# Kernel tuning notes

Measured on AMD Instinct MI355X. Metric: run time of the kernel, lower is better.

The kernel has to match this reference:

```python
import jax, jax.numpy as jnp
import numpy as np

B, LATENT, P, NUM_ATOMS, H, L, E = 16, 128, 16, 64, 64, 4, 32768
N = P * NUM_ATOMS  # 1024

def _lin(k, i, o, s=0.05):
    kw, kb = jax.random.split(k)
    return jax.random.normal(kw, (i, o), jnp.float32) * s, jax.random.normal(kb, (o,), jnp.float32) * s

def setup_inputs() -> dict:
    key = jax.random.key(0)
    ks = jax.random.split(key, 32)
    z = jax.random.normal(ks[0], (B, LATENT), jnp.float32)
    edge_index = jax.random.randint(ks[1], (2, E), 0, N, jnp.int32)
    # build_node_features: (frame/P, atom/num_atoms, 1) per node
    fr = jnp.repeat(jnp.arange(P), NUM_ATOMS) / P
    at = jnp.tile(jnp.arange(NUM_ATOMS), P) / NUM_ATOMS
    node_features = jnp.stack([fr, at, jnp.ones(N)], -1).astype(jnp.float32)
    Wg, bg = _lin(ks[2], LATENT, H)
    Wn, bn = _lin(ks[3], 3, H)
    def stack(fn, base):
        outs = [fn(jax.random.fold_in(key, base + l)) for l in range(L)]
        return tuple(jnp.stack(t) for t in zip(*outs))
    eW1, eb1 = stack(lambda k: _lin(k, 2 * H + 1, H), 100)
    eW2, eb2 = stack(lambda k: _lin(k, H, H), 200)
    cW1, cb1 = stack(lambda k: _lin(k, H, H), 300)
    cW2 = jnp.stack([jax.random.normal(jax.random.fold_in(key, 400 + l), (H, 1), jnp.float32) * 0.05 for l in range(L)])
    nW1, nb1 = stack(lambda k: _lin(k, 2 * H, H), 500)
    nW2, nb2 = stack(lambda k: _lin(k, H, H), 600)
    lng = jnp.ones((L, H), jnp.float32)
    lnb = jnp.zeros((L, H), jnp.float32)
    oW1, ob1 = _lin(ks[4], H, H)
    oW2, ob2 = _lin(ks[5], H, 3)
    return dict(z=z, edge_index=edge_index, node_features=node_features, Wg=Wg, bg=bg, Wn=Wn, bn=bn,
                eW1=eW1, eb1=eb1, eW2=eW2, eb2=eb2, cW1=cW1, cb1=cb1, cW2=cW2,
                nW1=nW1, nb1=nb1, nW2=nW2, nb2=nb2, lng=lng, lnb=lnb,
                oW1=oW1, ob1=ob1, oW2=oW2, ob2=ob2)

def _forward(z, edge_index, node_features, Wg, bg, Wn, bn, eW1, eb1, eW2, eb2,
             cW1, cb1, cW2, nW1, nb1, nW2, nb2, lng, lnb, oW1, ob1, oW2, ob2):
    b = z.shape[0]
    n = node_features.shape[0]
    row, col = edge_index[0], edge_index[1]  # aggregate messages to row
    counts = jnp.clip(jnp.zeros((n,), jnp.float32).at[row].add(1.0), 1.0, None)
    g = z @ Wg + bg                              # [B,H]
    h = (node_features @ Wn + bn)[None] + g[:, None]  # [B,N,H]
    pos = jnp.zeros((b, n, 3), h.dtype)
    for l in range(L):
        hi, hj = h[:, row], h[:, col]            # [B,E,H] gathers
        diff = pos[:, row] - pos[:, col]         # [B,E,3]
        d2 = jnp.sum(diff * diff, -1, keepdims=True)
        m = jax.nn.silu(jnp.concatenate([hi, hj, d2], -1) @ eW1[l] + eb1[l])
        m = jax.nn.silu(m @ eW2[l] + eb2[l])     # [B,E,H]
        w = jax.nn.silu(m @ cW1[l] + cb1[l]) @ cW2[l]  # [B,E,1]
        trans = diff * w
        pos = pos + jnp.zeros_like(pos).at[:, row].add(trans) / counts[None, :, None]
        agg = jnp.zeros_like(h).at[:, row].add(m)      # scatter-sum to nodes
        u = jax.nn.silu(jnp.concatenate([h, agg], -1) @ nW1[l] + nb1[l]) @ nW2[l] + nb2[l]
        h = h + u                                 # node residual
        mu = jnp.mean(h, -1, keepdims=True)
        var = jnp.mean((h - mu) ** 2, -1, keepdims=True)
        h = (h - mu) * jax.lax.rsqrt(var + 1e-5) * lng[l] + lnb[l]
    out = jax.nn.relu(h @ oW1 + ob1) @ oW2 + ob2   # [B,N,3]
    return out.reshape(b, -1)

def reference(z, edge_index, node_features, Wg, bg, Wn, bn, eW1, eb1, eW2, eb2,
              cW1, cb1, cW2, nW1, nb1, nW2, nb2, lng, lnb, oW1, ob1, oW2, ob2):
    return _forward(z, edge_index, node_features, Wg, bg, Wn, bn, eW1, eb1, eW2, eb2,
                    cW1, cb1, cW2, nW1, nb1, nW2, nb2, lng, lnb, oW1, ob1, oW2, ob2)
```

## Files before the change

### kernel.cpp

```cpp
#include <hip/hip_runtime.h>
#include <hip/hip_bf16.h>


namespace {

constexpr int kE = 32768, kLat = 128;

typedef __attribute__((ext_vector_type(8))) short short8;
typedef __attribute__((ext_vector_type(4))) float floatx4;

__device__ __forceinline__ unsigned short f2bf(float f){
  union { float f; unsigned int u; } v; v.f = f;
  unsigned int r = v.u + 0x7fffu + ((v.u >> 16) & 1u);
  return (unsigned short)(r >> 16);
}
__device__ __forceinline__ unsigned int packbf(float a, float b){
  return ((unsigned int)f2bf(b) << 16) | (unsigned int)f2bf(a);
}
__device__ __forceinline__ unsigned int pack2f(float a, float b){
  unsigned int ua = __float_as_uint(a) + 0x8000u;
  unsigned int ub = __float_as_uint(b) + 0x8000u;
  return __builtin_amdgcn_perm(ub, ua, 0x07060302);
}
__device__ __forceinline__ float bflo(unsigned int u){
  union { unsigned int u; float f; } v; v.u = u << 16; return v.f;
}
__device__ __forceinline__ float bfhi(unsigned int u){
  union { unsigned int u; float f; } v; v.u = u & 0xffff0000u; return v.f;
}
__device__ __forceinline__ float silu2(float x){
  float u = __builtin_amdgcn_exp2f(-1.44269504f * x);
  return x * __builtin_amdgcn_rcpf(1.0f + u);
}

__device__ __forceinline__ void gemm16g(const float* __restrict__ Wg,
                                        const float* Xl,
                                        int j0, int r0, float acc[4][4]){
  #pragma unroll 4
  for (int k = 0; k < 64; k++){
    float4 w = *(const float4*)(Wg + k*64 + j0);
    float4 x = *(const float4*)(Xl + k*20 + r0);
    float xv[4] = { x.x, x.y, x.z, x.w };
    float wv[4] = { w.x, w.y, w.z, w.w };
    #pragma unroll
    for (int i = 0; i < 4; i++)
      #pragma unroll
      for (int j = 0; j < 4; j++)
        acc[i][j] += xv[i]*wv[j];
  }
}

__global__ void k_scancnt(const int* ei, int* off, int* fill,
                          const float* z, const float* Wg, const float* bg,
                          float* g){
  __shared__ int s0[1024];
  __shared__ int s1[1024];
  int t = threadIdx.x;
  s0[t] = 0; fill[t] = 0;
  __syncthreads();
  #pragma unroll
  for (int i = 0; i < 32; i++) atomicAdd(&s0[ei[i*1024 + t]], 1);
  __syncthreads();
  int c = s0[t];
  int* src = s0; int* dst = s1;
  for (int o = 1; o < 1024; o <<= 1){
    int v = src[t] + ((t >= o) ? src[t-o] : 0);
    dst[t] = v; __syncthreads();
    int* tmp = src; src = dst; dst = tmp;
  }
  int inc = src[t];
  off[t] = inc - c;
  if (t == 1023) off[1024] = inc;
  int b = t >> 6, j = t & 63;
  float acc = bg[j];
  for (int k = 0; k < kLat; k++) acc += z[b*kLat + k] * Wg[k*64 + j];
  g[b*64 + j] = acc;
}

__global__ void k_bucket(const int* ei, const int* off, int* fill, int* ecol,
                         const float* eW2, unsigned short* wfragE,
                         const float* nf, const float* Wn, const float* bn,
                         const float* eW1, const float* eb1, const float* g,
                         float* An1, float* An2, float* Ag1, float* Ag2){
  __shared__ __align__(16) float W0[4096];
  __shared__ __align__(16) float W1[4096];
  __shared__ __align__(16) float HR[16*68];
  int tid = threadIdx.x, bid = blockIdx.x;
  int e = bid*256 + tid;
  int r = ei[e];
  int s = atomicAdd(&fill[r], 1);
  ecol[off[r] + s] = ei[kE + e];
  if (bid < 4){
    int l = bid;
    for (int i = tid; i < 4096; i += 256){
      int f = i >> 9, lane = (i >> 3) & 63, j8 = i & 7;
      int jt = f >> 1, ks = f & 1;
      int k = ks*32 + (lane >> 4)*8 + j8;
      int j = jt*16 + (lane & 15);
      wfragE[l*4096 + i] = f2bf(eW2[l*4096 + k*64 + j]);
    }
  } else if (bid < 68){
    const float4* e1a = (const float4*)(eW1);
    const float4* e1b = (const float4*)(eW1 + 4096);
    for (int i = tid; i < 1024; i += 256){
      ((float4*)W0)[i] = e1a[i]; ((float4*)W1)[i] = e1b[i];
    }
    int rl = tid >> 4, c = tid & 15, j0 = c*4;
    int n = (bid - 4)*16 + rl;
    float f0 = nf[n*3], f1 = nf[n*3+1], f2 = nf[n*3+2];
    float4 hv;
    hv.x = f0*Wn[j0+0] + f1*Wn[64+j0+0] + f2*Wn[128+j0+0] + bn[j0+0];
    hv.y = f0*Wn[j0+1] + f1*Wn[64+j0+1] + f2*Wn[128+j0+1] + bn[j0+1];
    hv.z = f0*Wn[j0+2] + f1*Wn[64+j0+2] + f2*Wn[128+j0+2] + bn[j0+2];
    hv.w = f0*Wn[j0+3] + f1*Wn[64+j0+3] + f2*Wn[128+j0+3] + bn[j0+3];
    *(float4*)(HR + rl*68 + j0) = hv;
    __syncthreads();
    float4 b1 = *(const float4*)(eb1 + j0);
    float a1[4] = { b1.x, b1.y, b1.z, b1.w };
    float a2[4] = { 0.f, 0.f, 0.f, 0.f };
    #pragma unroll 8
    for (int k = 0; k < 64; k++){
      float hk = HR[rl*68 + k];
      float4 w1 = *(const float4*)(W0 + k*64 + j0);
      float4 w2 = *(const float4*)(W1 + k*64 + j0);
      a1[0] += hk*w1.x; a1[1] += hk*w1.y; a1[2] += hk*w1.z; a1[3] += hk*w1.w;
      a2[0] += hk*w2.x; a2[1] += hk*w2.y; a2[2] += hk*w2.z; a2[3] += hk*w2.w;
    }
    float4 o1 = { a1[0], a1[1], a1[2], a1[3] };
    float4 o2 = { a2[0], a2[1], a2[2], a2[3] };
    *(float4*)(An1 + n*64 + j0) = o1;
    *(float4*)(An2 + n*64 + j0) = o2;
  } else if (bid == 68){
    int bb = tid >> 4, j0 = (tid & 15)*4;
    float a1[4] = {0.f,0.f,0.f,0.f}, a2[4] = {0.f,0.f,0.f,0.f};
    for (int k = 0; k < 64; k++){
      float gk = g[bb*64 + k];
      float4 w1 = *(const float4*)(eW1 + k*64 + j0);
      float4 w2 = *(const float4*)(eW1 + 4096 + k*64 + j0);
      a1[0] += gk*w1.x; a1[1] += gk*w1.y; a1[2] += gk*w1.z; a1[3] += gk*w1.w;
      a2[0] += gk*w2.x; a2[1] += gk*w2.y; a2[2] += gk*w2.z; a2[3] += gk*w2.w;
    }
    float4 o1 = { a1[0], a1[1], a1[2], a1[3] };
    float4 o2 = { a2[0], a2[1], a2[2], a2[3] };
    *(float4*)(Ag1 + bb*64 + j0) = o1;
    *(float4*)(Ag2 + bb*64 + j0) = o2;
  }
}

__global__ __launch_bounds__(256, 1) void k_pre1(const float* nf, const float* Wn,
      const float* bn, const float* g, const float* An1, const float* An2,
      const float* Ag1, const float* Ag2, float* h, float* A1,
      unsigned short* A2){
  int idx = blockIdx.x*256 + threadIdx.x;
  int row = idx >> 4;
  int j0  = (idx & 15) * 4;
  int n = row >> 4, bb = row & 15;
  float4 a1 = *(const float4*)(An1 + n*64 + j0);
  float4 g1 = *(const float4*)(Ag1 + bb*64 + j0);
  a1.x += g1.x; a1.y += g1.y; a1.z += g1.z; a1.w += g1.w;
  *(float4*)(A1 + row*64 + j0) = a1;
  float4 a2 = *(const float4*)(An2 + n*64 + j0);
  float4 g2 = *(const float4*)(Ag2 + bb*64 + j0);
  a2.x += g2.x; a2.y += g2.y; a2.z += g2.z; a2.w += g2.w;
  uint2 pk; pk.x = packbf(a2.x, a2.y); pk.y = packbf(a2.z, a2.w);
  *(uint2*)(A2 + row*64 + j0) = pk;
  float f0 = nf[n*3], f1 = nf[n*3+1], f2 = nf[n*3+2];
  float4 w0 = *(const float4*)(Wn + j0);
  float4 w1 = *(const float4*)(Wn + 64 + j0);
  float4 w2 = *(const float4*)(Wn + 128 + j0);
  float4 bv = *(const float4*)(bn + j0);
  float4 gv = *(const float4*)(g + bb*64 + j0);
  float4 hv;
  hv.x = f0*w0.x + f1*w1.x + f2*w2.x + bv.x + gv.x;
  hv.y = f0*w0.y + f1*w1.y + f2*w2.y + bv.y + gv.y;
  hv.z = f0*w0.z + f1*w1.z + f2*w2.z + bv.z + gv.z;
  hv.w = f0*w0.w + f1*w1.w + f2*w2.w + bv.w + gv.w;
  *(float4*)(h + (bb*1024 + n)*64 + j0) = hv;
}

template <bool LAST>
__global__ __launch_bounds__(256) void k_layer(int l,
      const float* A1r, const unsigned short* A2r,
      float* A1w, unsigned short* A2w,
      float* h, const unsigned short* wfragE, const float* eb2,
      const int* off, const int* ecol,
      const float* nW1, const float* nb1_, const float* nW2, const float* nb2_,
      const float* lng_, const float* lnb_, const float* eW1, const float* eb1_,
      const float* oW1, const float* ob1_, const float* oW2, const float* ob2_,
      float* out){
  __shared__ __align__(16) float XT[64*20];
  __shared__ __align__(16) float AGL[64*20];
  int tid = threadIdx.x, nd = blockIdx.x;
  int lane = tid & 63, wv = tid >> 6, m = lane & 15, quad = lane >> 4;

  for (int i = tid; i < 64*20; i += 256) AGL[i] = 0.f;
  __syncthreads();

  {
    short8 wf[8];
    #pragma unroll
    for (int f = 0; f < 8; f++)
      wf[f] = *(const short8*)(wfragE + l*4096 + f*512 + lane*8);
    floatx4 dini[4], agg[4];
    #pragma unroll
    for (int jt = 0; jt < 4; jt++){
      dini[jt] = *(const floatx4*)(eb2 + l*64 + jt*16 + quad*4);
      agg[jt] = (floatx4){0.f,0.f,0.f,0.f};
    }
    int e0 = off[nd] + wv, e1 = off[nd+1];
    if (e0 < e1){
      float4 a1[4];
      #pragma unroll
      for (int ks = 0; ks < 2; ks++){
        a1[ks*2+0] = *(const float4*)(A1r + (nd<<10) + (m<<6) + ks*32 + quad*8);
        a1[ks*2+1] = *(const float4*)(A1r + (nd<<10) + (m<<6) + ks*32 + quad*8 + 4);
      }
      int c0 = ecol[e0];
      uint4 p0 = *(const uint4*)(A2r + ((c0<<4)+m)*64 + quad*8);
      uint4 p1 = *(const uint4*)(A2r + ((c0<<4)+m)*64 + 32 + quad*8);
      for (int e = e0; e < e1; e += 4){
        uint4 c_0 = p0, c_1 = p1;
        if (e + 4 < e1){
          int cn = ecol[e+4];
          p0 = *(const uint4*)(A2r + ((cn<<4)+m)*64 + quad*8);
          p1 = *(const uint4*)(A2r + ((cn<<4)+m)*64 + 32 + quad*8);
        }
        short8 bfr[2];
        #pragma unroll
        for (int ks = 0; ks < 2; ks++){
          uint4 a2r = (ks == 0) ? c_0 : c_1;
          float4 x0 = a1[ks*2+0];
          float4 x1 = a1[ks*2+1];
          float v0 = silu2(x0.x + bflo(a2r.x));
          float v1 = silu2(x0.y + bfhi(a2r.x));
          float v2 = silu2(x0.z + bflo(a2r.y));
          float v3 = silu2(x0.w + bfhi(a2r.y));
          float v4 = silu2(x1.x + bflo(a2r.z));
          float v5 = silu2(x1.y + bfhi(a2r.z));
          float v6 = silu2(x1.z + bflo(a2r.w));
          float v7 = silu2(x1.w + bfhi(a2r.w));
          union { uint4 u; short8 s; } bu;
          bu.u.x = pack2f(v0, v1); bu.u.y = pack2f(v2, v3);
          bu.u.z = pack2f(v4, v5); bu.u.w = pack2f(v6, v7);
          bfr[ks] = bu.s;
        }
        #pragma unroll
        for (int jt = 0; jt < 4; jt++){
          floatx4 d = dini[jt];
          d = __builtin_amdgcn_mfma_f32_16x16x32_bf16(wf[jt*2+0], bfr[0], d, 0, 0, 0);
          d = __builtin_amdgcn_mfma_f32_16x16x32_bf16(wf[jt*2+1], bfr[1], d, 0, 0, 0);
          floatx4 a = agg[jt];
          a.x += silu2(d.x); a.y += silu2(d.y);
          a.z += silu2(d.z); a.w += silu2(d.w);
          agg[jt] = a;
        }
      }
    }
    #pragma unroll
    for (int jt = 0; jt < 4; jt++)
      #pragma unroll
      for (int i = 0; i < 4; i++)
        atomicAdd(&AGL[(jt*16 + quad*4 + i)*20 + m], agg[jt][i]);
  }
  __syncthreads();
  if (wv != 0) return;

  int c = tid & 15, gq = (tid >> 4) & 3;
  int j0 = c*4, r0 = gq*4;

  float hold[4][4];
  float acc[4][4];
  #pragma unroll
  for (int i = 0; i < 4; i++){
    int bb = r0 + i;
    float4 v = *(const float4*)(h + (bb*1024 + nd)*64 + j0);
    hold[i][0]=v.x; hold[i][1]=v.y; hold[i][2]=v.z; hold[i][3]=v.w;
  }
  #pragma unroll
  for (int j = 0; j < 4; j++){
    float4 t = { hold[0][j], hold[1][j], hold[2][j], hold[3][j] };
    *(float4*)(XT + (j0 + j)*20 + r0) = t;
  }
  { float4 b1 = *(const float4*)(nb1_ + l*64 + j0);
    float bv[4] = { b1.x, b1.y, b1.z, b1.w };
    #pragma unroll
    for (int i = 0; i < 4; i++)
      #pragma unroll
      for (int j = 0; j < 4; j++) acc[i][j] = bv[j]; }
  gemm16g(nW1 + l*8192, XT, j0, r0, acc);
  gemm16g(nW1 + l*8192 + 4096, AGL, j0, r0, acc);
  #pragma unroll
  for (int i = 0; i < 4; i++)
    #pragma unroll
    for (int j = 0; j < 4; j++) acc[i][j] = silu2(acc[i][j]);
  #pragma unroll
  for (int j = 0; j < 4; j++){
    float4 t = { acc[0][j], acc[1][j], acc[2][j], acc[3][j] };
    *(float4*)(XT + (j0 + j)*20 + r0) = t;
  }
  float u4[4][4];
  { float4 b2 = *(const float4*)(nb2_ + l*64 + j0);
    float bv[4] = { b2.x, b2.y, b2.z, b2.w };
    #pragma unroll
    for (int i = 0; i < 4; i++)
      #pragma unroll
      for (int j = 0; j < 4; j++) u4[i][j] = bv[j]; }
  gemm16g(nW2 + l*4096, XT, j0, r0, u4);
  float4 lgv = *(const float4*)(lng_ + l*64 + j0);
  float4 lbv = *(const float4*)(lnb_ + l*64 + j0);
  float hn[4][4];
  #pragma unroll
  for (int i = 0; i < 4; i++){
    float hv[4];
    #pragma unroll
    for (int j = 0; j < 4; j++) hv[j] = hold[i][j] + u4[i][j];
    float s1 = hv[0]+hv[1]+hv[2]+hv[3];
    float s2 = hv[0]*hv[0]+hv[1]*hv[1]+hv[2]*hv[2]+hv[3]*hv[3];
    s1 += __shfl_xor(s1, 1, 64); s1 += __shfl_xor(s1, 2, 64);
    s1 += __shfl_xor(s1, 4, 64); s1 += __shfl_xor(s1, 8, 64);
    s2 += __shfl_xor(s2, 1, 64); s2 += __shfl_xor(s2, 2, 64);
    s2 += __shfl_xor(s2, 4, 64); s2 += __shfl_xor(s2, 8, 64);
    float mu  = s1 * (1.0f/64.0f);
    float var = s2 * (1.0f/64.0f) - mu*mu;
    float rs  = rsqrtf(var + 1e-5f);
    hn[i][0] = (hv[0]-mu)*rs*lgv.x + lbv.x;
    hn[i][1] = (hv[1]-mu)*rs*lgv.y + lbv.y;
    hn[i][2] = (hv[2]-mu)*rs*lgv.z + lbv.z;
    hn[i][3] = (hv[3]-mu)*rs*lgv.w + lbv.w;
  }
  if (!LAST){
    #pragma unroll
    for (int i = 0; i < 4; i++){
      int bb = r0 + i;
      float4 v = { hn[i][0], hn[i][1], hn[i][2], hn[i][3] };
      *(float4*)(h + (bb*1024 + nd)*64 + j0) = v;
    }
    #pragma unroll
    for (int j = 0; j < 4; j++){
      float4 t = { hn[0][j], hn[1][j], hn[2][j], hn[3][j] };
      *(float4*)(XT + (j0 + j)*20 + r0) = t;
    }
    float a1r[4][4];
    { float4 b1 = *(const float4*)(eb1_ + (l+1)*64 + j0);
      float bv[4] = { b1.x, b1.y, b1.z, b1.w };
      #pragma unroll
      for (int i = 0; i < 4; i++)
        #pragma unroll
        for (int j = 0; j < 4; j++) a1r[i][j] = bv[j]; }
    gemm16g(eW1 + (l+1)*8256, XT, j0, r0, a1r);
    float a2r[4][4];
    #pragma unroll
    for (int i = 0; i < 4; i++)
      #pragma unroll
      for (int j = 0; j < 4; j++) a2r[i][j] = 0.f;
    gemm16g(eW1 + (l+1)*8256 + 4096, XT, j0, r0, a2r);
    #pragma unroll
    for (int i = 0; i < 4; i++){
      int bb = r0 + i;
      int tb = (nd*16 + bb)*64 + j0;
      float4 o1 = { a1r[i][0], a1r[i][1], a1r[i][2], a1r[i][3] };
      *(float4*)(A1w + tb) = o1;
      uint2 pk; pk.x = packbf(a2r[i][0], a2r[i][1]);
      pk.y = packbf(a2r[i][2], a2r[i][3]);
      *(uint2*)(A2w + tb) = pk;
    }
  } else {
    #pragma unroll
    for (int j = 0; j < 4; j++){
      float4 t = { hn[0][j], hn[1][j], hn[2][j], hn[3][j] };
      *(float4*)(XT + (j0 + j)*20 + r0) = t;
    }
    float tr[4][4];
    { float4 b1 = *(const float4*)(ob1_ + j0);
      float bv[4] = { b1.x, b1.y, b1.z, b1.w };
      #pragma unroll
      for (int i = 0; i < 4; i++)
        #pragma unroll
        for (int j = 0; j < 4; j++) tr[i][j] = bv[j]; }
    gemm16g(oW1, XT, j0, r0, tr);
    #pragma unroll
    for (int i = 0; i < 4; i++)
      #pragma unroll
      for (int j = 0; j < 4; j++) tr[i][j] = fmaxf(tr[i][j], 0.f);
    float po[4][3];
    #pragma unroll
    for (int i = 0; i < 4; i++){ po[i][0]=0.f; po[i][1]=0.f; po[i][2]=0.f; }
    #pragma unroll
    for (int j = 0; j < 4; j++){
      float w0 = oW2[(j0+j)*3 + 0];
      float w1 = oW2[(j0+j)*3 + 1];
      float w2 = oW2[(j0+j)*3 + 2];
      #pragma unroll
      for (int i = 0; i < 4; i++){
        po[i][0] += tr[i][j]*w0;
        po[i][1] += tr[i][j]*w1;
        po[i][2] += tr[i][j]*w2;
      }
    }
    #pragma unroll
    for (int i = 0; i < 4; i++)
      #pragma unroll
      for (int uu = 0; uu < 3; uu++){
        float v = po[i][uu];
        v += __shfl_xor(v, 1, 64); v += __shfl_xor(v, 2, 64);
        v += __shfl_xor(v, 4, 64); v += __shfl_xor(v, 8, 64);
        po[i][uu] = v;
      }
    if (c == 0){
      #pragma unroll
      for (int i = 0; i < 4; i++){
        int bb = r0 + i;
        out[bb*3072 + nd*3 + 0] = po[i][0] + ob2_[0];
        out[bb*3072 + nd*3 + 1] = po[i][1] + ob2_[1];
        out[bb*3072 + nd*3 + 2] = po[i][2] + ob2_[2];
      }
    }
  }
}

}

extern "C" void kernel_launch(void* const* d_in, const int* in_sizes, int n_in,
                              void* d_out, int out_size, void* d_ws, size_t ws_size,
                              hipStream_t stream){
  const float* z   = (const float*)d_in[0];
  const int*   ei  = (const int*)d_in[1];
  const float* nf  = (const float*)d_in[2];
  const float* Wg  = (const float*)d_in[3];  const float* bg  = (const float*)d_in[4];
  const float* Wn  = (const float*)d_in[5];  const float* bn  = (const float*)d_in[6];
  const float* eW1 = (const float*)d_in[7];  const float* eb1 = (const float*)d_in[8];
  const float* eW2 = (const float*)d_in[9];  const float* eb2 = (const float*)d_in[10];
  const float* nW1 = (const float*)d_in[14]; const float* nb1 = (const float*)d_in[15];
  const float* nW2 = (const float*)d_in[16]; const float* nb2 = (const float*)d_in[17];
  const float* lng = (const float*)d_in[18]; const float* lnb = (const float*)d_in[19];
  const float* oW1 = (const float*)d_in[20]; const float* ob1 = (const float*)d_in[21];
  const float* oW2 = (const float*)d_in[22]; const float* ob2 = (const float*)d_in[23];

  float* W      = (float*)d_ws;
  float* h      = W;
  float* A1a    = W + 1048576;
  float* A1b    = W + 2097152;
  unsigned short* A2a    = (unsigned short*)(W + 3145728);
  unsigned short* A2b    = (unsigned short*)(W + 3670016);
  unsigned short* wfragE = (unsigned short*)(W + 4194304);
  float* g      = W + 4202496;
  float* An1    = W + 4203520;
  float* An2    = W + 4269056;
  float* Ag1    = W + 4334592;
  float* Ag2    = W + 4335616;
  int*   off    = (int*)(W + 4336640);
  int*   fill   = off + 1025;
  int*   ecol   = fill + 1024;

  k_scancnt<<<1, 1024, 0, stream>>>(ei, off, fill, z, Wg, bg, g);
  k_bucket <<<128, 256, 0, stream>>>(ei, off, fill, ecol, eW2, wfragE,
                                     nf, Wn, bn, eW1, eb1, g, An1, An2, Ag1, Ag2);
  k_pre1   <<<1024,256, 0, stream>>>(nf, Wn, bn, g, An1, An2, Ag1, Ag2, h, A1a, A2a);

  for (int l = 0; l < 4; l++){
    const float* A1r = (l & 1) ? A1b : A1a;
    const unsigned short* A2r = (l & 1) ? A2b : A2a;
    float* A1w = (l & 1) ? A1a : A1b;
    unsigned short* A2w = (l & 1) ? A2a : A2b;
    if (l < 3)
      k_layer<false><<<1024, 256, 0, stream>>>(l, A1r, A2r, A1w, A2w, h, wfragE,
            eb2, off, ecol, nW1, nb1, nW2, nb2, lng, lnb, eW1, eb1,
            oW1, ob1, oW2, ob2, (float*)d_out);
    else
      k_layer<true> <<<1024, 256, 0, stream>>>(l, A1r, A2r, A1w, A2w, h, wfragE,
            eb2, off, ecol, nW1, nb1, nW2, nb2, lng, lnb, eW1, eb1,
            oW1, ob1, oW2, ob2, (float*)d_out);
  }
}
```

Baseline: 390.9 us.

## Spread node-update tail across all four wavefronts, one batch row per lane group

Previously only wavefront 0 ran the per-node MLP, layernorm and next-layer projection tail, each lane computing a 4x4 tile while the other waves exited. Now every wavefront takes part: each lane group owns one batch row (row = wave*4 + group) and computes a 1x4 output slice. This removes the serial tail where three quarters of the block sat idle. In exchange each lane reloads the weight float4 for every single row, so there is less register reuse and more weight-load traffic per FLOP.

```diff
diff --git a/kernel.cpp b/kernel.cpp
--- a/kernel.cpp
+++ b/kernel.cpp
@@ -33,20 +33,14 @@
   return x * __builtin_amdgcn_rcpf(1.0f + u);
 }
 
-__device__ __forceinline__ void gemm16g(const float* __restrict__ Wg,
-                                        const float* Xl,
-                                        int j0, int r0, float acc[4][4]){
+__device__ __forceinline__ void gemmR(const float* __restrict__ Wg,
+                                      const float* Xl, int j0, int row,
+                                      float acc[4]){
   #pragma unroll 4
   for (int k = 0; k < 64; k++){
     float4 w = *(const float4*)(Wg + k*64 + j0);
-    float4 x = *(const float4*)(Xl + k*20 + r0);
-    float xv[4] = { x.x, x.y, x.z, x.w };
-    float wv[4] = { w.x, w.y, w.z, w.w };
-    #pragma unroll
-    for (int i = 0; i < 4; i++)
-      #pragma unroll
-      for (int j = 0; j < 4; j++)
-        acc[i][j] += xv[i]*wv[j];
+    float x = Xl[k*20 + row];
+    acc[0] += x*w.x; acc[1] += x*w.y; acc[2] += x*w.z; acc[3] += x*w.w;
   }
 }
 
@@ -263,57 +257,38 @@
         atomicAdd(&AGL[(jt*16 + quad*4 + i)*20 + m], agg[jt][i]);
   }
   __syncthreads();
-  if (wv != 0) return;
-
-  int c = tid & 15, gq = (tid >> 4) & 3;
-  int j0 = c*4, r0 = gq*4;
-
-  float hold[4][4];
-  float acc[4][4];
+
+  int c = lane & 15, gq = (lane >> 4) & 3;
+  int j0 = c*4;
+  int row = wv*4 + gq;
+
+  float hold[4];
+  {
+    float4 v = *(const float4*)(h + (row*1024 + nd)*64 + j0);
+    hold[0]=v.x; hold[1]=v.y; hold[2]=v.z; hold[3]=v.w;
+  }
   #pragma unroll
-  for (int i = 0; i < 4; i++){
-    int bb = r0 + i;
-    float4 v = *(const float4*)(h + (bb*1024 + nd)*64 + j0);
-    hold[i][0]=v.x; hold[i][1]=v.y; hold[i][2]=v.z; hold[i][3]=v.w;
-  }
+  for (int jj = 0; jj < 4; jj++) XT[(j0 + jj)*20 + row] = hold[jj];
+  float acc[4];
+  { float4 b1 = *(const float4*)(nb1_ + l*64 + j0);
+    acc[0]=b1.x; acc[1]=b1.y; acc[2]=b1.z; acc[3]=b1.w; }
+  gemmR(nW1 + l*8192, XT, j0, row, acc);
+  gemmR(nW1 + l*8192 + 4096, AGL, j0, row, acc);
   #pragma unroll
-  for (int j = 0; j < 4; j++){
-    float4 t = { hold[0][j], hold[1][j], hold[2][j], hold[3][j] };
-    *(float4*)(XT + (j0 + j)*20 + r0) = t;
-  }
-  { float4 b1 = *(const float4*)(nb1_ + l*64 + j0);
-    float bv[4] = { b1.x, b1.y, b1.z, b1.w };
-    #pragma unroll
-    for (int i = 0; i < 4; i++)
-      #pragma unroll
-      for (int j = 0; j < 4; j++) acc[i][j] = bv[j]; }
-  gemm16g(nW1 + l*8192, XT, j0, r0, acc);
-  gemm16g(nW1 + l*8192 + 4096, AGL, j0, r0, acc);
+  for (int jj = 0; jj < 4; jj++) acc[jj] = silu2(acc[jj]);
   #pragma unroll
-  for (int i = 0; i < 4; i++)
-    #pragma unroll
-    for (int j = 0; j < 4; j++) acc[i][j] = silu2(acc[i][j]);
-  #pragma unroll
-  for (int j = 0; j < 4; j++){
-    float4 t = { acc[0][j], acc[1][j], acc[2][j], acc[3][j] };
-    *(float4*)(XT + (j0 + j)*20 + r0) = t;
-  }
-  float u4[4][4];
+  for (int jj = 0; jj < 4; jj++) XT[(j0 + jj)*20 + row] = acc[jj];
+  float u4[4];
   { float4 b2 = *(const float4*)(nb2_ + l*64 + j0);
-    float bv[4] = { b2.x, b2.y, b2.z, b2.w };
-    #pragma unroll
-    for (int i = 0; i < 4; i++)
-      #pragma unroll
-      for (int j = 0; j < 4; j++) u4[i][j] = bv[j]; }
-  gemm16g(nW2 + l*4096, XT, j0, r0, u4);
+    u4[0]=b2.x; u4[1]=b2.y; u4[2]=b2.z; u4[3]=b2.w; }
+  gemmR(nW2 + l*4096, XT, j0, row, u4);
   float4 lgv = *(const float4*)(lng_ + l*64 + j0);
   float4 lbv = *(const float4*)(lnb_ + l*64 + j0);
-  float hn[4][4];
-  #pragma unroll
-  for (int i = 0; i < 4; i++){
+  float hn[4];
+  {
     float hv[4];
     #pragma unroll
-    for (int j = 0; j < 4; j++) hv[j] = hold[i][j] + u4[i][j];
+    for (int jj = 0; jj < 4; jj++) hv[jj] = hold[jj] + u4[jj];
     float s1 = hv[0]+hv[1]+hv[2]+hv[3];
     float s2 = hv[0]*hv[0]+hv[1]*hv[1]+hv[2]*hv[2]+hv[3]*hv[3];
     s1 += __shfl_xor(s1, 1, 64); s1 += __shfl_xor(s1, 2, 64);
@@ -323,97 +298,56 @@
     float mu  = s1 * (1.0f/64.0f);
     float var = s2 * (1.0f/64.0f) - mu*mu;
     float rs  = rsqrtf(var + 1e-5f);
-    hn[i][0] = (hv[0]-mu)*rs*lgv.x + lbv.x;
-    hn[i][1] = (hv[1]-mu)*rs*lgv.y + lbv.y;
-    hn[i][2] = (hv[2]-mu)*rs*lgv.z + lbv.z;
-    hn[i][3] = (hv[3]-mu)*rs*lgv.w + lbv.w;
+    hn[0] = (hv[0]-mu)*rs*lgv.x + lbv.x;
+    hn[1] = (hv[1]-mu)*rs*lgv.y + lbv.y;
+    hn[2] = (hv[2]-mu)*rs*lgv.z + lbv.z;
+    hn[3] = (hv[3]-mu)*rs*lgv.w + lbv.w;
   }
   if (!LAST){
-    #pragma unroll
-    for (int i = 0; i < 4; i++){
-      int bb = r0 + i;
-      float4 v = { hn[i][0], hn[i][1], hn[i][2], hn[i][3] };
-      *(float4*)(h + (bb*1024 + nd)*64 + j0) = v;
-    }
-    #pragma unroll
-    for (int j = 0; j < 4; j++){
-      float4 t = { hn[0][j], hn[1][j], hn[2][j], hn[3][j] };
-      *(float4*)(XT + (j0 + j)*20 + r0) = t;
-    }
-    float a1r[4][4];
+    { float4 v = { hn[0], hn[1], hn[2], hn[3] };
+      *(float4*)(h + (row*1024 + nd)*64 + j0) = v; }
+    #pragma unroll
+    for (int jj = 0; jj < 4; jj++) XT[(j0 + jj)*20 + row] = hn[jj];
+    float a1r[4];
     { float4 b1 = *(const float4*)(eb1_ + (l+1)*64 + j0);
-      float bv[4] = { b1.x, b1.y, b1.z, b1.w };
-      #pragma unroll
-      for (int i = 0; i < 4; i++)
-        #pragma unroll
-        for (int j = 0; j < 4; j++) a1r[i][j] = bv[j]; }
-    gemm16g(eW1 + (l+1)*8256, XT, j0, r0, a1r);
-    float a2r[4][4];
-    #pragma unroll
-    for (int i = 0; i < 4; i++)
-      #pragma unroll
-      for (int j = 0; j < 4; j++) a2r[i][j] = 0.f;
-    gemm16g(eW1 + (l+1)*8256 + 4096, XT, j0, r0, a2r);
-    #pragma unroll
-    for (int i = 0; i < 4; i++){
-      int bb = r0 + i;
-      int tb = (nd*16 + bb)*64 + j0;
-      float4 o1 = { a1r[i][0], a1r[i][1], a1r[i][2], a1r[i][3] };
-      *(float4*)(A1w + tb) = o1;
-      uint2 pk; pk.x = packbf(a2r[i][0], a2r[i][1]);
-      pk.y = packbf(a2r[i][2], a2r[i][3]);
-      *(uint2*)(A2w + tb) = pk;
-    }
+      a1r[0]=b1.x; a1r[1]=b1.y; a1r[2]=b1.z; a1r[3]=b1.w; }
+    gemmR(eW1 + (l+1)*8256, XT, j0, row, a1r);
+    float a2r[4] = { 0.f, 0.f, 0.f, 0.f };
+    gemmR(eW1 + (l+1)*8256 + 4096, XT, j0, row, a2r);
+    int tb = (nd*16 + row)*64 + j0;
+    float4 o1 = { a1r[0], a1r[1], a1r[2], a1r[3] };
+    *(float4*)(A1w + tb) = o1;
+    uint2 pk; pk.x = packbf(a2r[0], a2r[1]);
+    pk.y = packbf(a2r[2], a2r[3]);
+    *(uint2*)(A2w + tb) = pk;
   } else {
     #pragma unroll
-    for (int j = 0; j < 4; j++){
-      float4 t = { hn[0][j], hn[1][j], hn[2][j], hn[3][j] };
-      *(float4*)(XT + (j0 + j)*20 + r0) = t;
-    }
-    float tr[4][4];
+    for (int jj = 0; jj < 4; jj++) XT[(j0 + jj)*20 + row] = hn[jj];
+    float tr[4];
     { float4 b1 = *(const float4*)(ob1_ + j0);
-      float bv[4] = { b1.x, b1.y, b1.z, b1.w };
-      #pragma unroll
-      for (int i = 0; i < 4; i++)
-        #pragma unroll
-        for (int j = 0; j < 4; j++) tr[i][j] = bv[j]; }
-    gemm16g(oW1, XT, j0, r0, tr);
-    #pragma unroll
-    for (int i = 0; i < 4; i++)
-      #pragma unroll
-      for (int j = 0; j < 4; j++) tr[i][j] = fmaxf(tr[i][j], 0.f);
-    float po[4][3];
-    #pragma unroll
-    for (int i = 0; i < 4; i++){ po[i][0]=0.f; po[i][1]=0.f; po[i][2]=0.f; }
-    #pragma unroll
-    for (int j = 0; j < 4; j++){
-      float w0 = oW2[(j0+j)*3 + 0];
-      float w1 = oW2[(j0+j)*3 + 1];
-      float w2 = oW2[(j0+j)*3 + 2];
-      #pragma unroll
-      for (int i = 0; i < 4; i++){
-        po[i][0] += tr[i][j]*w0;
-        po[i][1] += tr[i][j]*w1;
-        po[i][2] += tr[i][j]*w2;
-      }
-    }
-    #pragma unroll
-    for (int i = 0; i < 4; i++)
-      #pragma unroll
-      for (int uu = 0; uu < 3; uu++){
-        float v = po[i][uu];
-        v += __shfl_xor(v, 1, 64); v += __shfl_xor(v, 2, 64);
-        v += __shfl_xor(v, 4, 64); v += __shfl_xor(v, 8, 64);
-        po[i][uu] = v;
-      }
+      tr[0]=b1.x; tr[1]=b1.y; tr[2]=b1.z; tr[3]=b1.w; }
+    gemmR(oW1, XT, j0, row, tr);
+    #pragma unroll
+    for (int jj = 0; jj < 4; jj++) tr[jj] = fmaxf(tr[jj], 0.f);
+    float po[3] = { 0.f, 0.f, 0.f };
+    #pragma unroll
+    for (int jj = 0; jj < 4; jj++){
+      float w0 = oW2[(j0+jj)*3 + 0];
+      float w1 = oW2[(j0+jj)*3 + 1];
+      float w2 = oW2[(j0+jj)*3 + 2];
+      po[0] += tr[jj]*w0; po[1] += tr[jj]*w1; po[2] += tr[jj]*w2;
+    }
+    #pragma unroll
+    for (int uu = 0; uu < 3; uu++){
+      float v = po[uu];
+      v += __shfl_xor(v, 1, 64); v += __shfl_xor(v, 2, 64);
+      v += __shfl_xor(v, 4, 64); v += __shfl_xor(v, 8, 64);
+      po[uu] = v;
+    }
     if (c == 0){
-      #pragma unroll
-      for (int i = 0; i < 4; i++){
-        int bb = r0 + i;
-        out[bb*3072 + nd*3 + 0] = po[i][0] + ob2_[0];
-        out[bb*3072 + nd*3 + 1] = po[i][1] + ob2_[1];
-        out[bb*3072 + nd*3 + 2] = po[i][2] + ob2_[2];
-      }
+      out[row*3072 + nd*3 + 0] = po[0] + ob2_[0];
+      out[row*3072 + nd*3 + 1] = po[1] + ob2_[1];
+      out[row*3072 + nd*3 + 2] = po[2] + ob2_[2];
     }
   }
 }
```

Result: slower. 501.8 us (+28.4%).

## Split layer kernel into edge and node-update kernels with LDS-staged weights

Applied to the files above, without the earlier changes.

The fused per-node layer kernel is split into an edge-aggregation kernel that writes per-node aggregates to a global buffer, and a node-update kernel that processes four nodes per block with all 256 threads. The node kernel stages each 64x64 weight matrix into shared memory and reuses it across 64 rows, where previously one wave per node read the weights from global memory. This is meant to raise weight reuse and thread utilisation in the node MLP, layernorm and next-layer projection. The cost is an extra launch per layer, a global round trip for the aggregates, and more barriers and shared memory.

```diff
diff --git a/kernel.cpp b/kernel.cpp
--- a/kernel.cpp
+++ b/kernel.cpp
@@ -33,13 +33,20 @@
   return x * __builtin_amdgcn_rcpf(1.0f + u);
 }
 
-__device__ __forceinline__ void gemm16g(const float* __restrict__ Wg,
-                                        const float* Xl,
-                                        int j0, int r0, float acc[4][4]){
+__device__ __forceinline__ void stage16k(float* Wl, const float* src, int tid){
+  const float4* p = (const float4*)src;
+  float4* d = (float4*)Wl;
+  d[tid]       = p[tid];
+  d[tid + 256] = p[tid + 256];
+  d[tid + 512] = p[tid + 512];
+  d[tid + 768] = p[tid + 768];
+}
+__device__ __forceinline__ void gemm64(const float* Wl, const float* Xl,
+                                       int j0, int r0, float acc[4][4]){
   #pragma unroll 4
   for (int k = 0; k < 64; k++){
-    float4 w = *(const float4*)(Wg + k*64 + j0);
-    float4 x = *(const float4*)(Xl + k*20 + r0);
+    float4 w = *(const float4*)(Wl + k*64 + j0);
+    float4 x = *(const float4*)(Xl + k*68 + r0);
     float xv[4] = { x.x, x.y, x.z, x.w };
     float wv[4] = { w.x, w.y, w.z, w.w };
     #pragma unroll
@@ -178,24 +185,16 @@
   *(float4*)(h + (bb*1024 + n)*64 + j0) = hv;
 }
 
-template <bool LAST>
-__global__ __launch_bounds__(256) void k_layer(int l,
+__global__ __launch_bounds__(256) void k_edge(int l,
       const float* A1r, const unsigned short* A2r,
-      float* A1w, unsigned short* A2w,
-      float* h, const unsigned short* wfragE, const float* eb2,
-      const int* off, const int* ecol,
-      const float* nW1, const float* nb1_, const float* nW2, const float* nb2_,
-      const float* lng_, const float* lnb_, const float* eW1, const float* eb1_,
-      const float* oW1, const float* ob1_, const float* oW2, const float* ob2_,
-      float* out){
-  __shared__ __align__(16) float XT[64*20];
+      const unsigned short* wfragE, const float* eb2,
+      const int* off, const int* ecol, float* AG){
   __shared__ __align__(16) float AGL[64*20];
   int tid = threadIdx.x, nd = blockIdx.x;
   int lane = tid & 63, wv = tid >> 6, m = lane & 15, quad = lane >> 4;
 
   for (int i = tid; i < 64*20; i += 256) AGL[i] = 0.f;
   __syncthreads();
-
   {
     short8 wf[8];
     #pragma unroll
@@ -263,32 +262,61 @@
         atomicAdd(&AGL[(jt*16 + quad*4 + i)*20 + m], agg[jt][i]);
   }
   __syncthreads();
-  if (wv != 0) return;
-
-  int c = tid & 15, gq = (tid >> 4) & 3;
+  int f = tid >> 2, b4 = (tid & 3) * 4;
+  float4 v = *(const float4*)(AGL + f*20 + b4);
+  *(float4*)(AG + nd*1024 + f*16 + b4) = v;
+}
+
+template <bool LAST>
+__global__ __launch_bounds__(256) void k_post(int l,
+      const float* AG, float* h, float* A1w, unsigned short* A2w,
+      const float* nW1, const float* nb1_, const float* nW2, const float* nb2_,
+      const float* lng_, const float* lnb_, const float* eW1, const float* eb1_,
+      const float* oW1, const float* ob1_, const float* oW2, const float* ob2_,
+      float* out){
+  __shared__ __align__(16) float W[4096];
+  __shared__ __align__(16) float XT[64*68];
+  __shared__ __align__(16) float AGT[64*68];
+  __shared__ float W2o[192];
+  __shared__ float ob2s[4];
+  int tid = threadIdx.x, bid = blockIdx.x;
+  int n0 = bid * 4;
+  int c = tid & 15, gq = tid >> 4;
   int j0 = c*4, r0 = gq*4;
 
-  float hold[4][4];
+  stage16k(W, nW1 + l*8192, tid);
+  for (int i = tid; i < 1024; i += 256){
+    int f4 = i >> 6, rr = i & 63;
+    int q = rr >> 4, b = rr & 15;
+    float4 v = *(const float4*)(h + (b*1024 + n0 + q)*64 + f4*4);
+    XT[(f4*4+0)*68 + rr] = v.x;
+    XT[(f4*4+1)*68 + rr] = v.y;
+    XT[(f4*4+2)*68 + rr] = v.z;
+    XT[(f4*4+3)*68 + rr] = v.w;
+  }
+  for (int i = tid; i < 1024; i += 256){
+    int q = i >> 8, j = i & 255, f = j >> 2, b4 = (j & 3)*4;
+    float4 v = *(const float4*)(AG + (n0+q)*1024 + f*16 + b4);
+    *(float4*)(AGT + f*68 + q*16 + b4) = v;
+  }
   float acc[4][4];
-  #pragma unroll
-  for (int i = 0; i < 4; i++){
-    int bb = r0 + i;
-    float4 v = *(const float4*)(h + (bb*1024 + nd)*64 + j0);
-    hold[i][0]=v.x; hold[i][1]=v.y; hold[i][2]=v.z; hold[i][3]=v.w;
-  }
-  #pragma unroll
-  for (int j = 0; j < 4; j++){
-    float4 t = { hold[0][j], hold[1][j], hold[2][j], hold[3][j] };
-    *(float4*)(XT + (j0 + j)*20 + r0) = t;
-  }
   { float4 b1 = *(const float4*)(nb1_ + l*64 + j0);
     float bv[4] = { b1.x, b1.y, b1.z, b1.w };
     #pragma unroll
     for (int i = 0; i < 4; i++)
       #pragma unroll
       for (int j = 0; j < 4; j++) acc[i][j] = bv[j]; }
-  gemm16g(nW1 + l*8192, XT, j0, r0, acc);
-  gemm16g(nW1 + l*8192 + 4096, AGL, j0, r0, acc);
+  __syncthreads();
+  gemm64(W, XT, j0, r0, acc);
+  float hold[4][4];
+  #pragma unroll
+  for (int i = 0; i < 4; i++)
+    #pragma unroll
+    for (int j = 0; j < 4; j++) hold[i][j] = XT[(j0+j)*68 + r0+i];
+  __syncthreads();
+  stage16k(W, nW1 + l*8192 + 4096, tid);
+  __syncthreads();
+  gemm64(W, AGT, j0, r0, acc);
   #pragma unroll
   for (int i = 0; i < 4; i++)
     #pragma unroll
@@ -296,8 +324,11 @@
   #pragma unroll
   for (int j = 0; j < 4; j++){
     float4 t = { acc[0][j], acc[1][j], acc[2][j], acc[3][j] };
-    *(float4*)(XT + (j0 + j)*20 + r0) = t;
-  }
+    *(float4*)(XT + (j0 + j)*68 + r0) = t;
+  }
+  __syncthreads();
+  stage16k(W, nW2 + l*4096, tid);
+  __syncthreads();
   float u4[4][4];
   { float4 b2 = *(const float4*)(nb2_ + l*64 + j0);
     float bv[4] = { b2.x, b2.y, b2.z, b2.w };
@@ -305,7 +336,7 @@
     for (int i = 0; i < 4; i++)
       #pragma unroll
       for (int j = 0; j < 4; j++) u4[i][j] = bv[j]; }
-  gemm16g(nW2 + l*4096, XT, j0, r0, u4);
+  gemm64(W, XT, j0, r0, u4);
   float4 lgv = *(const float4*)(lng_ + l*64 + j0);
   float4 lbv = *(const float4*)(lnb_ + l*64 + j0);
   float hn[4][4];
@@ -328,17 +359,20 @@
     hn[i][2] = (hv[2]-mu)*rs*lgv.z + lbv.z;
     hn[i][3] = (hv[3]-mu)*rs*lgv.w + lbv.w;
   }
+  __syncthreads();
   if (!LAST){
+    stage16k(W, eW1 + (l+1)*8256, tid);
     #pragma unroll
     for (int i = 0; i < 4; i++){
-      int bb = r0 + i;
+      int rr = r0 + i;
+      int q = rr >> 4, b = rr & 15;
       float4 v = { hn[i][0], hn[i][1], hn[i][2], hn[i][3] };
-      *(float4*)(h + (bb*1024 + nd)*64 + j0) = v;
+      *(float4*)(h + (b*1024 + n0 + q)*64 + j0) = v;
     }
     #pragma unroll
     for (int j = 0; j < 4; j++){
       float4 t = { hn[0][j], hn[1][j], hn[2][j], hn[3][j] };
-      *(float4*)(XT + (j0 + j)*20 + r0) = t;
+      *(float4*)(XT + (j0 + j)*68 + r0) = t;
     }
     float a1r[4][4];
     { float4 b1 = *(const float4*)(eb1_ + (l+1)*64 + j0);
@@ -347,17 +381,22 @@
       for (int i = 0; i < 4; i++)
         #pragma unroll
         for (int j = 0; j < 4; j++) a1r[i][j] = bv[j]; }
-    gemm16g(eW1 + (l+1)*8256, XT, j0, r0, a1r);
+    __syncthreads();
+    gemm64(W, XT, j0, r0, a1r);
+    __syncthreads();
+    stage16k(W, eW1 + (l+1)*8256 + 4096, tid);
     float a2r[4][4];
     #pragma unroll
     for (int i = 0; i < 4; i++)
       #pragma unroll
       for (int j = 0; j < 4; j++) a2r[i][j] = 0.f;
-    gemm16g(eW1 + (l+1)*8256 + 4096, XT, j0, r0, a2r);
+    __syncthreads();
+    gemm64(W, XT, j0, r0, a2r);
     #pragma unroll
     for (int i = 0; i < 4; i++){
-      int bb = r0 + i;
-      int tb = (nd*16 + bb)*64 + j0;
+      int rr = r0 + i;
+      int q = rr >> 4, b = rr & 15;
+      int tb = ((n0+q)*16 + b)*64 + j0;
       float4 o1 = { a1r[i][0], a1r[i][1], a1r[i][2], a1r[i][3] };
       *(float4*)(A1w + tb) = o1;
       uint2 pk; pk.x = packbf(a2r[i][0], a2r[i][1]);
@@ -365,10 +404,13 @@
       *(uint2*)(A2w + tb) = pk;
     }
   } else {
+    stage16k(W, oW1, tid);
+    if (tid < 192) W2o[tid] = oW2[tid];
+    if (tid < 3)   ob2s[tid] = ob2_[tid];
     #pragma unroll
     for (int j = 0; j < 4; j++){
       float4 t = { hn[0][j], hn[1][j], hn[2][j], hn[3][j] };
-      *(float4*)(XT + (j0 + j)*20 + r0) = t;
+      *(float4*)(XT + (j0 + j)*68 + r0) = t;
     }
     float tr[4][4];
     { float4 b1 = *(const float4*)(ob1_ + j0);
@@ -377,7 +419,8 @@
       for (int i = 0; i < 4; i++)
         #pragma unroll
         for (int j = 0; j < 4; j++) tr[i][j] = bv[j]; }
-    gemm16g(oW1, XT, j0, r0, tr);
+    __syncthreads();
+    gemm64(W, XT, j0, r0, tr);
     #pragma unroll
     for (int i = 0; i < 4; i++)
       #pragma unroll
@@ -387,9 +430,9 @@
     for (int i = 0; i < 4; i++){ po[i][0]=0.f; po[i][1]=0.f; po[i][2]=0.f; }
     #pragma unroll
     for (int j = 0; j < 4; j++){
-      float w0 = oW2[(j0+j)*3 + 0];
-      float w1 = oW2[(j0+j)*3 + 1];
-      float w2 = oW2[(j0+j)*3 + 2];
+      float w0 = W2o[(j0+j)*3 + 0];
+      float w1 = W2o[(j0+j)*3 + 1];
+      float w2 = W2o[(j0+j)*3 + 2];
       #pragma unroll
       for (int i = 0; i < 4; i++){
         po[i][0] += tr[i][j]*w0;
@@ -409,10 +452,11 @@
     if (c == 0){
       #pragma unroll
       for (int i = 0; i < 4; i++){
-        int bb = r0 + i;
-        out[bb*3072 + nd*3 + 0] = po[i][0] + ob2_[0];
-        out[bb*3072 + nd*3 + 1] = po[i][1] + ob2_[1];
-        out[bb*3072 + nd*3 + 2] = po[i][2] + ob2_[2];
+        int rr = r0 + i;
+        int q = rr >> 4, b = rr & 15;
+        out[b*3072 + (n0+q)*3 + 0] = po[i][0] + ob2s[0];
+        out[b*3072 + (n0+q)*3 + 1] = po[i][1] + ob2s[1];
+        out[b*3072 + (n0+q)*3 + 2] = po[i][2] + ob2s[2];
       }
     }
   }
@@ -451,6 +495,7 @@
   int*   off    = (int*)(W + 4336640);
   int*   fill   = off + 1025;
   int*   ecol   = fill + 1024;
+  float* AG     = W + 4372480;
 
   k_scancnt<<<1, 1024, 0, stream>>>(ei, off, fill, z, Wg, bg, g);
   k_bucket <<<128, 256, 0, stream>>>(ei, off, fill, ecol, eW2, wfragE,
@@ -462,13 +507,14 @@
     const unsigned short* A2r = (l & 1) ? A2b : A2a;
     float* A1w = (l & 1) ? A1a : A1b;
     unsigned short* A2w = (l & 1) ? A2a : A2b;
+    k_edge<<<1024, 256, 0, stream>>>(l, A1r, A2r, wfragE, eb2, off, ecol, AG);
     if (l < 3)
-      k_layer<false><<<1024, 256, 0, stream>>>(l, A1r, A2r, A1w, A2w, h, wfragE,
-            eb2, off, ecol, nW1, nb1, nW2, nb2, lng, lnb, eW1, eb1,
+      k_post<false><<<256, 256, 0, stream>>>(l, AG, h, A1w, A2w,
+            nW1, nb1, nW2, nb2, lng, lnb, eW1, eb1,
             oW1, ob1, oW2, ob2, (float*)d_out);
     else
-      k_layer<true> <<<1024, 256, 0, stream>>>(l, A1r, A2r, A1w, A2w, h, wfragE,
-            eb2, off, ecol, nW1, nb1, nW2, nb2, lng, lnb, eW1, eb1,
+      k_post<true> <<<256, 256, 0, stream>>>(l, AG, h, A1w, A2w,
+            nW1, nb1, nW2, nb2, lng, lnb, eW1, eb1,
             oW1, ob1, oW2, ob2, (float*)d_out);
   }
 }
```

After: 378.2 us. 3.3% less time.
